# Performance work log

Hardware: AMD Instinct MI355X
Metric: run time of the kernel (lower is better)

Reference implementation:

```python
import jax, jax.numpy as jnp
import numpy as np

B, T, D, H, O = 1024, 2048, 13, 128, 2


def setup_inputs() -> dict:
    key = jax.random.key(0)
    k1, k2, k3, k4 = jax.random.split(key, 4)
    xs = jax.random.normal(k1, (B, T, D), dtype=jnp.float32)
    # nn.Linear(in, out, bias=False) weights: [out, in]
    W_in = jax.random.normal(k2, (H, D), dtype=jnp.float32) / np.sqrt(D).astype(np.float32)
    W_h = jax.random.normal(k3, (H, H), dtype=jnp.float32) / np.sqrt(H).astype(np.float32)
    W_out = jax.random.normal(k4, (O, H), dtype=jnp.float32) / np.sqrt(H).astype(np.float32)
    return {"xs": xs, "W_in": W_in, "W_h": W_h, "W_out": W_out}


def reference(xs, W_in, W_h, W_out):
    # Vanilla hardtanh RNN, h0 = 0 (first step y = hardtanh(in_h(x)) == hardtanh(in_h(x) + W_h @ 0)).
    # Precompute all input projections in one big GEMM: [B, T, H]
    pre = jnp.einsum('btd,hd->bth', xs, W_in)

    def step(h, xh_t):  # h: [B, H], xh_t: [B, H]
        h = jnp.clip(xh_t + h @ W_h.T, -1.0, 1.0)  # F.hardtanh
        return h, None

    h0 = jnp.zeros((xs.shape[0], W_in.shape[0]), dtype=xs.dtype)
    hT, _ = jax.lax.scan(step, h0, jnp.swapaxes(pre, 0, 1))  # scan over time
    # Only the final hidden state per sequence is projected to the output.
    return hT @ W_out.T  # [B, O]
```

## Files before the change

kernel.cpp:

```cpp
#include <hip/hip_runtime.h>
#include <stdint.h>


#define RNN_B 1024
#define RNN_T 2048
#define RNN_D 13
#define RNN_H 128
#define RNN_O 2

#define NB 16
#define NWAVE 4
#define NTHR (NWAVE * 64)
#define ROWS 136

using f32x4 = __attribute__((ext_vector_type(4))) float;
using v8s   = __attribute__((ext_vector_type(8))) short;

__device__ __forceinline__ short f2bf(float f) {
    union { float f; uint32_t u; } c; c.f = f;
    uint32_t u = c.u + 0x7fffu + ((c.u >> 16) & 1u);
    return (short)(u >> 16);
}
__device__ __forceinline__ float bf2fs(short s) {
    union { uint32_t u; float f; } c; c.u = ((uint32_t)(uint16_t)s) << 16;
    return c.f;
}
__device__ __forceinline__ float bitf(uint32_t u) {
    union { uint32_t u; float f; } c; c.u = u; return c.f;
}
__device__ __forceinline__ uint32_t cvtpk(float a, float b) {
    uint32_t r;
    asm("v_cvt_pk_bf16_f32 %0, %1, %2" : "=v"(r) : "v"(a), "v"(b));
    return r;
}
__device__ __forceinline__ v8s pack4(uint32_t a, uint32_t b, uint32_t c, uint32_t d) {
    union { uint32_t u[4]; v8s s; } z;
    z.u[0] = a; z.u[1] = b; z.u[2] = c; z.u[3] = d; return z.s;
}
__device__ __forceinline__ float clamp1(float v) {
    return __builtin_amdgcn_fmed3f(v, -1.0f, 1.0f);
}

__device__ __forceinline__ void barrier_lgkm() {
    __builtin_amdgcn_sched_barrier(0);
    asm volatile("s_waitcnt lgkmcnt(0)" ::: "memory");
    __builtin_amdgcn_s_barrier();
    asm volatile("" ::: "memory");
    __builtin_amdgcn_sched_barrier(0);
}

#define MFMA(a, b, c) __builtin_amdgcn_mfma_f32_16x16x32_bf16((a), (b), (c), 0, 0, 0)

#define STEP(CUR, NXT, X0, X1, X2, X3, TPF)                                      \
  do {                                                                           \
           \
    v8s bh1 = *(const v8s*)&Hhi[CUR][n][ktq1 + g8];                              \
    v8s bl1 = *(const v8s*)&Hlo[CUR][n][ktq1 + g8];                              \
    v8s bh2 = *(const v8s*)&Hhi[CUR][n][ktq2 + g8];                              \
    v8s bl2 = *(const v8s*)&Hlo[CUR][n][ktq2 + g8];                              \
    v8s bh3 = *(const v8s*)&Hhi[CUR][n][ktq3 + g8];                              \
    v8s bl3 = *(const v8s*)&Hlo[CUR][n][ktq3 + g8];                              \
                                \
    float m0 = X0, m1 = X1, m2 = X2, m3 = X3;                                    \
    if (g == 3) { m1 = 0.0f; m2 = 0.0f; m3 = 0.0f; }                             \
    uint32_t xh01 = cvtpk(m0, m1), xh23 = cvtpk(m2, m3);                         \
    float q0 = m0 - bitf(xh01 << 16);                                            \
    float q1 = m1 - bitf(xh01 & 0xffff0000u);                                    \
    float q2 = m2 - bitf(xh23 << 16);                                            \
    float q3 = m3 - bitf(xh23 & 0xffff0000u);                                    \
    uint32_t xl01 = cvtpk(q0, q1), xl23 = cvtpk(q2, q3);                         \
    v8s xh = pack4(xh01, xh23, 0u, 0u);                                          \
    v8s xl = pack4(xl01, xl23, 0u, 0u);                                          \
                    \
    f32x4 Z = {0.f, 0.f, 0.f, 0.f};                                              \
    f32x4 A1 = MFMA(whiA[4], xh, Z);                                             \
    f32x4 A2 = MFMA(whiA[4], xl, Z);                                             \
    f32x4 A3 = MFMA(wloA[4], xh, Z);                                             \
    A1 = MFMA(whiA[0], selfBh, A1);                                              \
    A2 = MFMA(whiA[0], selfBl, A2);                                              \
    A3 = MFMA(wloA[0], selfBh, A3);                                              \
             \
    if ((TPF) < RNN_T) {                                                         \
      const float* xp = xrow + (size_t)(TPF) * RNN_D;                            \
      X0 = xp[d0]; X1 = xp[d1]; X2 = xp[d2]; X3 = xp[d3];                        \
    }                                                                            \
    A1 = MFMA(whiA[1], bh1, A1);                                                 \
    A2 = MFMA(whiA[1], bl1, A2);                                                 \
    A3 = MFMA(wloA[1], bh1, A3);                                                 \
    A1 = MFMA(whiA[2], bh2, A1);                                                 \
    A2 = MFMA(whiA[2], bl2, A2);                                                 \
    A3 = MFMA(wloA[2], bh2, A3);                                                 \
    A1 = MFMA(whiA[3], bh3, A1);                                                 \
    A2 = MFMA(whiA[3], bl3, A2);                                                 \
    A3 = MFMA(wloA[3], bh3, A3);                                                 \
                 \
    f32x4 B1 = MFMA(whiB[4], xh, Z);                                             \
    f32x4 B2 = MFMA(whiB[4], xl, Z);                                             \
    f32x4 B3 = MFMA(wloB[4], xh, Z);                                             \
    B1 = MFMA(whiB[0], selfBh, B1);                                              \
    B2 = MFMA(whiB[0], selfBl, B2);                                              \
    B3 = MFMA(wloB[0], selfBh, B3);                                              \
    float v0 = clamp1(A1[0] + A2[0] + A3[0]);                                    \
    float v1 = clamp1(A1[1] + A2[1] + A3[1]);                                    \
    float v2 = clamp1(A1[2] + A2[2] + A3[2]);                                    \
    float v3 = clamp1(A1[3] + A2[3] + A3[3]);                                    \
    B1 = MFMA(whiB[1], bh1, B1);                                                 \
    B2 = MFMA(whiB[1], bl1, B2);                                                 \
    B3 = MFMA(wloB[1], bh1, B3);                                                 \
    uint32_t h01A = cvtpk(v0, v1), h23A = cvtpk(v2, v3);                         \
    float p0 = v0 - bitf(h01A << 16);                                            \
    float p1 = v1 - bitf(h01A & 0xffff0000u);                                    \
    float p2 = v2 - bitf(h23A << 16);                                            \
    float p3 = v3 - bitf(h23A & 0xffff0000u);                                    \
    B1 = MFMA(whiB[2], bh2, B1);                                                 \
    B2 = MFMA(whiB[2], bl2, B2);                                                 \
    B3 = MFMA(wloB[2], bh2, B3);                                                 \
    uint32_t l01A = cvtpk(p0, p1), l23A = cvtpk(p2, p3);                         \
    {                                                                            \
      int2 wv; wv.x = (int)h01A; wv.y = (int)h23A;                               \
      *(int2*)&Hhi[NXT][n][wbase + g8] = wv;                                     \
      wv.x = (int)l01A; wv.y = (int)l23A;                                        \
      *(int2*)&Hlo[NXT][n][wbase + g8] = wv;                                     \
    }                                                                            \
    B1 = MFMA(whiB[3], bh3, B1);                                                 \
    B2 = MFMA(whiB[3], bl3, B2);                                                 \
    B3 = MFMA(wloB[3], bh3, B3);                                                 \
                                     \
    {                                                                            \
      float w0 = clamp1(B1[0] + B2[0] + B3[0]);                                  \
      float w1 = clamp1(B1[1] + B2[1] + B3[1]);                                  \
      float w2 = clamp1(B1[2] + B2[2] + B3[2]);                                  \
      float w3 = clamp1(B1[3] + B2[3] + B3[3]);                                  \
      uint32_t h01B = cvtpk(w0, w1), h23B = cvtpk(w2, w3);                       \
      float r0 = w0 - bitf(h01B << 16);                                          \
      float r1 = w1 - bitf(h01B & 0xffff0000u);                                  \
      float r2 = w2 - bitf(h23B << 16);                                          \
      float r3 = w3 - bitf(h23B & 0xffff0000u);                                  \
      uint32_t l01B = cvtpk(r0, r1), l23B = cvtpk(r2, r3);                       \
      selfBh = pack4(h01A, h23A, h01B, h23B);                                    \
      selfBl = pack4(l01A, l23A, l01B, l23B);                                    \
      int2 wv; wv.x = (int)h01B; wv.y = (int)h23B;                               \
      *(int2*)&Hhi[NXT][n][wbase + g8 + 4] = wv;                                 \
      wv.x = (int)l01B; wv.y = (int)l23B;                                        \
      *(int2*)&Hlo[NXT][n][wbase + g8 + 4] = wv;                                 \
    }                                                                            \
    barrier_lgkm();                                                              \
  } while (0)

__global__ __launch_bounds__(NTHR, 1) void rnn_mfma12_kernel(
    const float* __restrict__ xs,
    const float* __restrict__ W_in,
    const float* __restrict__ W_h,
    const float* __restrict__ W_out,
    float* __restrict__ out)
{
    __shared__ __align__(16) short Hhi[2][NB][ROWS];
    __shared__ __align__(16) short Hlo[2][NB][ROWS];

    const int tid  = threadIdx.x;
    const int lane = tid & 63;
    const int wid  = tid >> 6;
    const int n    = lane & 15;
    const int g    = lane >> 4;
    const int g8   = g * 8;
    const int wbase = 32 * wid;
    const int b0   = blockIdx.x * NB;

    const int ktq1 = ((wid + 1) & 3) * 32;
    const int ktq2 = ((wid + 2) & 3) * 32;
    const int ktq3 = ((wid + 3) & 3) * 32;

    const int d0 = (4 * g + 0 > 12) ? 12 : 4 * g + 0;
    const int d1 = (4 * g + 1 > 12) ? 12 : 4 * g + 1;
    const int d2 = (4 * g + 2 > 12) ? 12 : 4 * g + 2;
    const int d3 = (4 * g + 3 > 12) ? 12 : 4 * g + 3;

    v8s whiA[5], wloA[5], whiB[5], wloB[5];
    #pragma unroll
    for (int mi = 0; mi < 2; ++mi) {
        const int row = 16 * (wid * 2 + mi) + n;
        #pragma unroll
        for (int q = 0; q < 4; ++q) {
            const int kt = (wid + q) & 3;
            v8s h8, l8;
            #pragma unroll
            for (int j = 0; j < 4; ++j) {
                const float w1 = W_h[row * RNN_H + 32 * kt + 4 * g + j];
                const float w2 = W_h[row * RNN_H + 32 * kt + 16 + 4 * g + j];
                const short h1 = f2bf(w1);
                const short h2 = f2bf(w2);
                h8[j] = h1; h8[4 + j] = h2;
                l8[j] = f2bf(w1 - bf2fs(h1));
                l8[4 + j] = f2bf(w2 - bf2fs(h2));
            }
            if (mi == 0) { whiA[q] = h8; wloA[q] = l8; }
            else         { whiB[q] = h8; wloB[q] = l8; }
        }
        {
            v8s h8, l8;
            #pragma unroll
            for (int j = 0; j < 4; ++j) {
                const int kx = 4 * g + j;
                const float w1 = (kx < RNN_D) ? W_in[row * RNN_D + kx] : 0.0f;
                const short h1 = f2bf(w1);
                h8[j] = h1; h8[4 + j] = 0;
                l8[j] = f2bf(w1 - bf2fs(h1));
                l8[4 + j] = 0;
            }
            if (mi == 0) { whiA[4] = h8; wloA[4] = l8; }
            else         { whiB[4] = h8; wloB[4] = l8; }
        }
    }

    for (int idx = tid; idx < NB * ROWS; idx += NTHR) {
        (&Hhi[0][0][0])[idx] = 0;
        (&Hlo[0][0][0])[idx] = 0;
    }

    v8s selfBh = {0, 0, 0, 0, 0, 0, 0, 0};
    v8s selfBl = {0, 0, 0, 0, 0, 0, 0, 0};

    const float* xrow = xs + (size_t)(b0 + n) * RNN_T * RNN_D;
    float xa0 = xrow[d0], xa1 = xrow[d1], xa2 = xrow[d2], xa3 = xrow[d3];
    float xb0 = xrow[RNN_D + d0], xb1 = xrow[RNN_D + d1];
    float xb2 = xrow[RNN_D + d2], xb3 = xrow[RNN_D + d3];
    __syncthreads();

    for (int t = 0; t < RNN_T; t += 2) {
        STEP(0, 1, xa0, xa1, xa2, xa3, t + 2);
        STEP(1, 0, xb0, xb1, xb2, xb3, t + 3);
    }

    __syncthreads();

    if (wid == 0 && lane < NB * RNN_O) {
        const int nn = lane & 15;
        const int o  = lane >> 4;
        float acc = 0.0f;
        for (int i = 0; i < RNN_H; ++i) {
            const int pos = 32 * (i >> 5) + 8 * ((i >> 2) & 3)
                          + 4 * ((i >> 4) & 1) + (i & 3);
            const float hv = bf2fs(Hhi[0][nn][pos]) + bf2fs(Hlo[0][nn][pos]);
            acc = fmaf(W_out[o * RNN_H + i], hv, acc);
        }
        out[(size_t)(b0 + nn) * RNN_O + o] = acc;
    }
}

extern "C" void kernel_launch(void* const* d_in, const int* in_sizes, int n_in,
                              void* d_out, int out_size, void* d_ws, size_t ws_size,
                              hipStream_t stream) {
    const float* xs    = (const float*)d_in[0];
    const float* W_in  = (const float*)d_in[1];
    const float* W_h   = (const float*)d_in[2];
    const float* W_out = (const float*)d_in[3];
    float* out = (float*)d_out;

    rnn_mfma12_kernel<<<RNN_B / NB, NTHR, 0, stream>>>(xs, W_in, W_h, W_out, out);
}
```

Measured before the change: 1.211 ms.

## Replace per-step block barrier with per-wave LDS flag spin-waits

Drops the workgroup barrier at the end of each recurrence step. Each wave now publishes its completed step in a shared-memory flag and spins only on the three peer waves whose hidden-state slices it reads. The input-projection MFMAs and the next x prefetch are moved ahead of the wait so they can overlap with waiting, and the A/B MFMA chains are interleaved. This trades a full barrier for point-to-point dependencies that let waves drift up to one step apart, at the cost of volatile spin loops on LDS.

```diff
diff --git a/kernel.cpp b/kernel.cpp
--- a/kernel.cpp
+++ b/kernel.cpp
@@ -41,26 +41,11 @@
     return __builtin_amdgcn_fmed3f(v, -1.0f, 1.0f);
 }
 
-__device__ __forceinline__ void barrier_lgkm() {
-    __builtin_amdgcn_sched_barrier(0);
-    asm volatile("s_waitcnt lgkmcnt(0)" ::: "memory");
-    __builtin_amdgcn_s_barrier();
-    asm volatile("" ::: "memory");
-    __builtin_amdgcn_sched_barrier(0);
-}
-
 #define MFMA(a, b, c) __builtin_amdgcn_mfma_f32_16x16x32_bf16((a), (b), (c), 0, 0, 0)
 
-#define STEP(CUR, NXT, X0, X1, X2, X3, TPF)                                      \
+#define STEP(CUR, NXT, X0, X1, X2, X3, TPF, TCUR)                                \
   do {                                                                           \
-           \
-    v8s bh1 = *(const v8s*)&Hhi[CUR][n][ktq1 + g8];                              \
-    v8s bl1 = *(const v8s*)&Hlo[CUR][n][ktq1 + g8];                              \
-    v8s bh2 = *(const v8s*)&Hhi[CUR][n][ktq2 + g8];                              \
-    v8s bl2 = *(const v8s*)&Hlo[CUR][n][ktq2 + g8];                              \
-    v8s bh3 = *(const v8s*)&Hhi[CUR][n][ktq3 + g8];                              \
-    v8s bl3 = *(const v8s*)&Hlo[CUR][n][ktq3 + g8];                              \
-                                \
+               \
     float m0 = X0, m1 = X1, m2 = X2, m3 = X3;                                    \
     if (g == 3) { m1 = 0.0f; m2 = 0.0f; m3 = 0.0f; }                             \
     uint32_t xh01 = cvtpk(m0, m1), xh23 = cvtpk(m2, m3);                         \
@@ -71,50 +56,71 @@
     uint32_t xl01 = cvtpk(q0, q1), xl23 = cvtpk(q2, q3);                         \
     v8s xh = pack4(xh01, xh23, 0u, 0u);                                          \
     v8s xl = pack4(xl01, xl23, 0u, 0u);                                          \
-                    \
+                               \
     f32x4 Z = {0.f, 0.f, 0.f, 0.f};                                              \
     f32x4 A1 = MFMA(whiA[4], xh, Z);                                             \
+    f32x4 B1 = MFMA(whiB[4], xh, Z);                                             \
     f32x4 A2 = MFMA(whiA[4], xl, Z);                                             \
+    f32x4 B2 = MFMA(whiB[4], xl, Z);                                             \
     f32x4 A3 = MFMA(wloA[4], xh, Z);                                             \
-    A1 = MFMA(whiA[0], selfBh, A1);                                              \
-    A2 = MFMA(whiA[0], selfBl, A2);                                              \
-    A3 = MFMA(wloA[0], selfBh, A3);                                              \
-             \
+    f32x4 B3 = MFMA(wloB[4], xh, Z);                                             \
+               \
     if ((TPF) < RNN_T) {                                                         \
       const float* xp = xrow + (size_t)(TPF) * RNN_D;                            \
       X0 = xp[d0]; X1 = xp[d1]; X2 = xp[d2]; X3 = xp[d3];                        \
     }                                                                            \
+                               \
+    {                                                                            \
+      volatile int* vf = hflag;                                                  \
+      const int need = (TCUR) - 1;                                               \
+      while (vf[wq1] < need) {}                                                  \
+      while (vf[wq2] < need) {}                                                  \
+      while (vf[wq3] < need) {}                                                  \
+      asm volatile("" ::: "memory");                                             \
+    }                                                                            \
+                                       \
+    v8s bh1 = *(const v8s*)&Hhi[CUR][n][ktq1 + g8];                              \
+    v8s bl1 = *(const v8s*)&Hlo[CUR][n][ktq1 + g8];                              \
+    v8s bh2 = *(const v8s*)&Hhi[CUR][n][ktq2 + g8];                              \
+    v8s bl2 = *(const v8s*)&Hlo[CUR][n][ktq2 + g8];                              \
+    v8s bh3 = *(const v8s*)&Hhi[CUR][n][ktq3 + g8];                              \
+    v8s bl3 = *(const v8s*)&Hlo[CUR][n][ktq3 + g8];                              \
+                          \
+    A1 = MFMA(whiA[0], selfBh, A1);                                              \
+    B1 = MFMA(whiB[0], selfBh, B1);                                              \
+    A2 = MFMA(whiA[0], selfBl, A2);                                              \
+    B2 = MFMA(whiB[0], selfBl, B2);                                              \
+    A3 = MFMA(wloA[0], selfBh, A3);                                              \
+    B3 = MFMA(wloB[0], selfBh, B3);                                              \
+                                 \
     A1 = MFMA(whiA[1], bh1, A1);                                                 \
+    B1 = MFMA(whiB[1], bh1, B1);                                                 \
     A2 = MFMA(whiA[1], bl1, A2);                                                 \
+    B2 = MFMA(whiB[1], bl1, B2);                                                 \
     A3 = MFMA(wloA[1], bh1, A3);                                                 \
+    B3 = MFMA(wloB[1], bh1, B3);                                                 \
     A1 = MFMA(whiA[2], bh2, A1);                                                 \
+    B1 = MFMA(whiB[2], bh2, B1);                                                 \
     A2 = MFMA(whiA[2], bl2, A2);                                                 \
+    B2 = MFMA(whiB[2], bl2, B2);                                                 \
     A3 = MFMA(wloA[2], bh2, A3);                                                 \
+    B3 = MFMA(wloB[2], bh2, B3);                                                 \
     A1 = MFMA(whiA[3], bh3, A1);                                                 \
     A2 = MFMA(whiA[3], bl3, A2);                                                 \
     A3 = MFMA(wloA[3], bh3, A3);                                                 \
-                 \
-    f32x4 B1 = MFMA(whiB[4], xh, Z);                                             \
-    f32x4 B2 = MFMA(whiB[4], xl, Z);                                             \
-    f32x4 B3 = MFMA(wloB[4], xh, Z);                                             \
-    B1 = MFMA(whiB[0], selfBh, B1);                                              \
-    B2 = MFMA(whiB[0], selfBl, B2);                                              \
-    B3 = MFMA(wloB[0], selfBh, B3);                                              \
+                    \
     float v0 = clamp1(A1[0] + A2[0] + A3[0]);                                    \
     float v1 = clamp1(A1[1] + A2[1] + A3[1]);                                    \
     float v2 = clamp1(A1[2] + A2[2] + A3[2]);                                    \
     float v3 = clamp1(A1[3] + A2[3] + A3[3]);                                    \
-    B1 = MFMA(whiB[1], bh1, B1);                                                 \
-    B2 = MFMA(whiB[1], bl1, B2);                                                 \
-    B3 = MFMA(wloB[1], bh1, B3);                                                 \
+    B1 = MFMA(whiB[3], bh3, B1);                                                 \
+    B2 = MFMA(whiB[3], bl3, B2);                                                 \
+    B3 = MFMA(wloB[3], bh3, B3);                                                 \
     uint32_t h01A = cvtpk(v0, v1), h23A = cvtpk(v2, v3);                         \
     float p0 = v0 - bitf(h01A << 16);                                            \
     float p1 = v1 - bitf(h01A & 0xffff0000u);                                    \
     float p2 = v2 - bitf(h23A << 16);                                            \
     float p3 = v3 - bitf(h23A & 0xffff0000u);                                    \
-    B1 = MFMA(whiB[2], bh2, B1);                                                 \
-    B2 = MFMA(whiB[2], bl2, B2);                                                 \
-    B3 = MFMA(wloB[2], bh2, B3);                                                 \
     uint32_t l01A = cvtpk(p0, p1), l23A = cvtpk(p2, p3);                         \
     {                                                                            \
       int2 wv; wv.x = (int)h01A; wv.y = (int)h23A;                               \
@@ -122,10 +128,7 @@
       wv.x = (int)l01A; wv.y = (int)l23A;                                        \
       *(int2*)&Hlo[NXT][n][wbase + g8] = wv;                                     \
     }                                                                            \
-    B1 = MFMA(whiB[3], bh3, B1);                                                 \
-    B2 = MFMA(whiB[3], bl3, B2);                                                 \
-    B3 = MFMA(wloB[3], bh3, B3);                                                 \
-                                     \
+                   \
     {                                                                            \
       float w0 = clamp1(B1[0] + B2[0] + B3[0]);                                  \
       float w1 = clamp1(B1[1] + B2[1] + B3[1]);                                  \
@@ -144,10 +147,12 @@
       wv.x = (int)l01B; wv.y = (int)l23B;                                        \
       *(int2*)&Hlo[NXT][n][wbase + g8 + 4] = wv;                                 \
     }                                                                            \
-    barrier_lgkm();                                                              \
+                            \
+    asm volatile("s_waitcnt lgkmcnt(0)" ::: "memory");                           \
+    if (lane == 0) { volatile int* vf = hflag; vf[wid] = (TCUR); }               \
   } while (0)
 
-__global__ __launch_bounds__(NTHR, 1) void rnn_mfma12_kernel(
+__global__ __launch_bounds__(NTHR, 1) void rnn_mfma16_kernel(
     const float* __restrict__ xs,
     const float* __restrict__ W_in,
     const float* __restrict__ W_h,
@@ -156,6 +161,7 @@
 {
     __shared__ __align__(16) short Hhi[2][NB][ROWS];
     __shared__ __align__(16) short Hlo[2][NB][ROWS];
+    __shared__ int hflag[NWAVE];
 
     const int tid  = threadIdx.x;
     const int lane = tid & 63;
@@ -166,9 +172,8 @@
     const int wbase = 32 * wid;
     const int b0   = blockIdx.x * NB;
 
-    const int ktq1 = ((wid + 1) & 3) * 32;
-    const int ktq2 = ((wid + 2) & 3) * 32;
-    const int ktq3 = ((wid + 3) & 3) * 32;
+    const int wq1 = (wid + 1) & 3, wq2 = (wid + 2) & 3, wq3 = (wid + 3) & 3;
+    const int ktq1 = wq1 * 32, ktq2 = wq2 * 32, ktq3 = wq3 * 32;
 
     const int d0 = (4 * g + 0 > 12) ? 12 : 4 * g + 0;
     const int d1 = (4 * g + 1 > 12) ? 12 : 4 * g + 1;
@@ -216,6 +221,7 @@
         (&Hhi[0][0][0])[idx] = 0;
         (&Hlo[0][0][0])[idx] = 0;
     }
+    if (tid < NWAVE) hflag[tid] = -1;
 
     v8s selfBh = {0, 0, 0, 0, 0, 0, 0, 0};
     v8s selfBl = {0, 0, 0, 0, 0, 0, 0, 0};
@@ -227,8 +233,8 @@
     __syncthreads();
 
     for (int t = 0; t < RNN_T; t += 2) {
-        STEP(0, 1, xa0, xa1, xa2, xa3, t + 2);
-        STEP(1, 0, xb0, xb1, xb2, xb3, t + 3);
+        STEP(0, 1, xa0, xa1, xa2, xa3, t + 2, t);
+        STEP(1, 0, xb0, xb1, xb2, xb3, t + 3, t + 1);
     }
 
     __syncthreads();
@@ -256,5 +262,5 @@
     const float* W_out = (const float*)d_in[3];
     float* out = (float*)d_out;
 
-    rnn_mfma12_kernel<<<RNN_B / NB, NTHR, 0, stream>>>(xs, W_in, W_h, W_out, out);
-}
+    rnn_mfma16_kernel<<<RNN_B / NB, NTHR, 0, stream>>>(xs, W_in, W_h, W_out, out);
+}
```

After: 1.758 ms. +45.1%, slower.
